# Kernel tuning notes

Hardware: AMD Instinct MI355X
Metric: run time of the kernel (lower is better)

Reference implementation:

```python
import jax, jax.numpy as jnp
import numpy as np

C = 256
CQK = C // 8  # query/key channel dim from Conv3d(in, in//8, 1)


def setup_inputs() -> dict:
    key = jax.random.key(0)
    ks = jax.random.split(key, 8)
    B, D, H, W = 2, 16, 16, 16
    x = jax.random.normal(ks[0], (B, C, D, H, W), dtype=jnp.float32)
    s = 1.0 / np.sqrt(C)
    q_w = jax.random.normal(ks[1], (CQK, C), dtype=jnp.float32) * s
    q_b = jax.random.normal(ks[2], (CQK,), dtype=jnp.float32) * 0.01
    k_w = jax.random.normal(ks[3], (CQK, C), dtype=jnp.float32) * s
    k_b = jax.random.normal(ks[4], (CQK,), dtype=jnp.float32) * 0.01
    v_w = jax.random.normal(ks[5], (C, C), dtype=jnp.float32) * s
    v_b = jax.random.normal(ks[6], (C,), dtype=jnp.float32) * 0.01
    gamma = jax.random.normal(ks[7], (1,), dtype=jnp.float32)
    return {"x": x, "q_w": q_w, "q_b": q_b, "k_w": k_w, "k_b": k_b,
            "v_w": v_w, "v_b": v_b, "gamma": gamma}


def reference(x, q_w, q_b, k_w, k_b, v_w, v_b, gamma):
    B, Cc, D, H, W = x.shape
    N = D * H * W
    xf = x.reshape(B, Cc, N)  # [B, C, N]
    # 1x1x1 Conv3d == channel-mixing matmul
    q = jnp.einsum('oc,bcn->bon', q_w, xf) + q_b[None, :, None]  # [B, C/8, N]
    k = jnp.einsum('oc,bcn->bon', k_w, xf) + k_b[None, :, None]  # [B, C/8, N]
    v = jnp.einsum('oc,bcn->bon', v_w, xf) + v_b[None, :, None]  # [B, C, N]
    # attention[b, i, j] = sum_c q[b, c, i] * k[b, c, j]
    attn = jnp.einsum('bci,bcj->bij', q, k)  # [B, N, N]
    attn = jax.nn.softmax(attn, axis=-1)
    # out[b, c, i] = sum_j v[b, c, j] * attn[b, i, j]
    out = jnp.einsum('bcj,bij->bci', v, attn)  # [B, C, N]
    out = out.reshape(B, Cc, D, H, W)
    return gamma[0] * out + x
```

## Files before the change

### kernel.cpp

```cpp
#include <hip/hip_runtime.h>

#define C_DIM 256
#define CQK   32
#define N_DIM 4096
#define B_DIM 2

typedef __attribute__((ext_vector_type(8))) short bf16x8;
typedef __attribute__((ext_vector_type(4))) float f32x4;

__device__ __forceinline__ unsigned short f2bf(float f) {
    union { float f; unsigned u; } v; v.f = f;
    unsigned r = v.u + 0x7FFFu + ((v.u >> 16) & 1u);
    return (unsigned short)(r >> 16);
}
__device__ __forceinline__ unsigned pk2(float a, float b) {
    return (unsigned)f2bf(a) | ((unsigned)f2bf(b) << 16);
}
__device__ __forceinline__ unsigned pk2t(float a, float b) {
    union { float f; unsigned u; } ua, ub; ua.f = a; ub.f = b;
    return __builtin_amdgcn_perm(ub.u, ua.u, 0x07060302u);
}
#define EXP2(x) __builtin_amdgcn_exp2f(x)
#define MFMA(A, B, C) __builtin_amdgcn_mfma_f32_16x16x32_bf16((A), (B), (C), 0, 0, 0)

__global__ __launch_bounds__(256) void wconv(
    const float* __restrict__ q_w, const float* __restrict__ q_b,
    const float* __restrict__ k_w, const float* __restrict__ k_b,
    const float* __restrict__ v_w, const float* __restrict__ v_b,
    unsigned short* __restrict__ wbf, float* __restrict__ biasf)
{
    const float LOG2E = 1.4426950408889634f;
    int o = blockIdx.x, c = threadIdx.x;
    float w;
    if (o < 32)       w = q_w[o * C_DIM + c] * LOG2E;
    else if (o < 64)  w = k_w[(o - 32) * C_DIM + c];
    else              w = v_w[(o - 64) * C_DIM + c];
    wbf[o * C_DIM + c] = f2bf(w);
    if (c == 0) biasf[o] = (o < 32) ? q_b[o] * LOG2E
                         : (o < 64) ? k_b[o - 32] : v_b[o - 64];
}

__global__ __launch_bounds__(256, 2) void qkv_proj(
    const float* __restrict__ x, const unsigned short* __restrict__ wbf,
    const float* __restrict__ biasf,
    unsigned short* __restrict__ qT, unsigned short* __restrict__ kT,
    unsigned short* __restrict__ vbf)
{
    __shared__ __align__(16) unsigned short xsT[16 * 264];
    __shared__ __align__(16) unsigned short qkbuf[2][16 * 36];
    __shared__ __align__(16) unsigned short vbb[256 * 20];
    const int t  = threadIdx.x;
    const int b  = blockIdx.x >> 8;
    const int n0 = (blockIdx.x & 255) * 16;

    {
        int n4 = t & 3, cq = t >> 2;
        const float* xp = x + ((size_t)(b * C_DIM + cq * 4)) * N_DIM + n0 + n4 * 4;
        float4 r0 = *(const float4*)xp;
        float4 r1 = *(const float4*)(xp + N_DIM);
        float4 r2 = *(const float4*)(xp + 2 * N_DIM);
        float4 r3 = *(const float4*)(xp + 3 * N_DIM);
        float a0[4], a1[4], a2[4], a3[4];
        *(float4*)a0 = r0; *(float4*)a1 = r1; *(float4*)a2 = r2; *(float4*)a3 = r3;
        #pragma unroll
        for (int k = 0; k < 4; ++k) {
            uint2 pw;
            pw.x = pk2(a0[k], a1[k]);
            pw.y = pk2(a2[k], a3[k]);
            *(uint2*)&xsT[(n4 * 4 + k) * 264 + cq * 4] = pw;
        }
    }
    __syncthreads();

    const int w = t >> 6, lid = t & 63, lr = lid & 15, lq = lid >> 4;
    f32x4 acc[5] = {};
    #pragma unroll
    for (int ks = 0; ks < 8; ++ks) {
        bf16x8 xb = *(const bf16x8*)&xsT[lr * 264 + ks * 32 + lq * 8];
        #pragma unroll
        for (int u = 0; u < 5; ++u) {
            int gm = w * 5 + u;
            bf16x8 af = *(const bf16x8*)&wbf[(gm * 16 + lr) * C_DIM + ks * 32 + lq * 8];
            acc[u] = MFMA(af, xb, acc[u]);
        }
    }
    #pragma unroll
    for (int u = 0; u < 5; ++u) {
        int gm = w * 5 + u;
        float bv[4];
        *(float4*)bv = *(const float4*)&biasf[gm * 16 + lq * 4];
        if (gm >= 4) {
            int vc = (gm - 4) * 16 + lq * 4;
            #pragma unroll
            for (int r = 0; r < 4; ++r)
                vbb[(vc + r) * 20 + lr] = f2bf(acc[u][r] + bv[r]);
        } else {
            int sel = gm >> 1, half = gm & 1;
            uint2 pw;
            pw.x = pk2(acc[u][0] + bv[0], acc[u][1] + bv[1]);
            pw.y = pk2(acc[u][2] + bv[2], acc[u][3] + bv[3]);
            *(uint2*)&qkbuf[sel][lr * 36 + half * 16 + lq * 4] = pw;
        }
    }
    __syncthreads();
    if (t < 128) {
        int sel = t >> 6, idx = t & 63;
        int n = idx >> 2, ch8 = (idx & 3) * 8;
        const unsigned short* src = &qkbuf[sel][n * 36 + ch8];
        uint2 a = *(const uint2*)src;
        uint2 c = *(const uint2*)(src + 4);
        unsigned short* dst = (sel ? kT : qT) + ((size_t)b * N_DIM + n0 + n) * CQK + ch8;
        uint4 st; st.x = a.x; st.y = a.y; st.z = c.x; st.w = c.y;
        *(uint4*)dst = st;
    }
    {
        const unsigned short* src = &vbb[t * 20];
        uint2 a = *(const uint2*)(src + 0);
        uint2 bq = *(const uint2*)(src + 4);
        uint2 c = *(const uint2*)(src + 8);
        uint2 d = *(const uint2*)(src + 12);
        unsigned short* dst = vbf + ((size_t)b * C_DIM + t) * N_DIM + n0;
        uint4 s0; s0.x = a.x; s0.y = a.y; s0.z = bq.x; s0.w = bq.y;
        uint4 s1; s1.x = c.x; s1.y = c.y; s1.z = d.x; s1.w = d.y;
        *(uint4*)dst = s0;
        *(uint4*)(dst + 8) = s1;
    }
}

__global__ __launch_bounds__(256, 2) void attn_kernel(
    const unsigned short* __restrict__ qT, const unsigned short* __restrict__ kT,
    const unsigned short* __restrict__ vbf, const float* __restrict__ x,
    const float* __restrict__ gamma, float* __restrict__ out)
{
    __shared__ __align__(16) char smem[40960 + 1536];
    unsigned short* pbase = (unsigned short*)smem;
    float* obuf = (float*)smem;
    float* lbuf = (float*)(smem + 40960);

    const int t  = threadIdx.x;
    const int b  = blockIdx.x >> 8;
    const int qt = (blockIdx.x >> 2) & 63;
    const int cs = blockIdx.x & 3;
    const int i0 = qt * 64, c0 = cs * 64;
    const int w = t >> 6, lid = t & 63, lr = lid & 15, lq = lid >> 4;

    const unsigned short* qTb = qT + (size_t)b * N_DIM * CQK;
    const unsigned short* kTb = kT + (size_t)b * N_DIM * CQK;
    const unsigned short* vb  = vbf + (size_t)b * C_DIM * N_DIM;

    unsigned short* pW0 = pbase + (w * 2 + 0) * (64 * 40);
    unsigned short* pW1 = pbase + (w * 2 + 1) * (64 * 40);

    bf16x8 bq[4];
    #pragma unroll
    for (int it = 0; it < 4; ++it)
        bq[it] = *(const bf16x8*)&qTb[(i0 + it * 16 + lr) * CQK + lq * 8];

    f32x4 oa[4][4] = {};
    float lp[4] = {};

    const int jwbase = w * 1024;

    bf16x8 akc0 = *(const bf16x8*)&kTb[(jwbase + lr) * CQK + lq * 8];
    bf16x8 akc1 = *(const bf16x8*)&kTb[(jwbase + 16 + lr) * CQK + lq * 8];
    bf16x8 avU[4];

    {
        #pragma unroll
        for (int ct = 0; ct < 4; ++ct)
            avU[ct] = *(const bf16x8*)&vb[(size_t)(c0 + ct * 16 + lr) * N_DIM + jwbase + lq * 8];
        bf16x8 akn0 = *(const bf16x8*)&kTb[(jwbase + 32 + lr) * CQK + lq * 8];
        bf16x8 akn1 = *(const bf16x8*)&kTb[(jwbase + 32 + 16 + lr) * CQK + lq * 8];
        const f32x4 z = {};
        #pragma unroll
        for (int it = 0; it < 4; ++it) {
            f32x4 s0 = MFMA(akc0, bq[it], z);
            f32x4 s1 = MFMA(akc1, bq[it], z);
            float e0 = EXP2(s0[0]), e1 = EXP2(s0[1]), e2 = EXP2(s0[2]), e3 = EXP2(s0[3]);
            float f0 = EXP2(s1[0]), f1 = EXP2(s1[1]), f2 = EXP2(s1[2]), f3 = EXP2(s1[3]);
            lp[it] += ((e0 + e1) + (e2 + e3)) + ((f0 + f1) + (f2 + f3));
            uint2 pw0; pw0.x = pk2t(e0, e1); pw0.y = pk2t(e2, e3);
            uint2 pw1; pw1.x = pk2t(f0, f1); pw1.y = pk2t(f2, f3);
            unsigned short* prow = pW0 + (it * 16 + lr) * 40;
            *(uint2*)&prow[lq * 4]      = pw0;
            *(uint2*)&prow[16 + lq * 4] = pw1;
        }
        akc0 = akn0; akc1 = akn1;
    }

    #pragma unroll 2
    for (int k = 1; k < 32; ++k) {
        const int j0 = jwbase + k * 32;
        const int jn = jwbase + ((k + 1) & 31) * 32;
        bf16x8 avI[4];
        #pragma unroll
        for (int ct = 0; ct < 4; ++ct)
            avI[ct] = *(const bf16x8*)&vb[(size_t)(c0 + ct * 16 + lr) * N_DIM + j0 + lq * 8];
        bf16x8 akn0 = *(const bf16x8*)&kTb[(jn + lr) * CQK + lq * 8];
        bf16x8 akn1 = *(const bf16x8*)&kTb[(jn + 16 + lr) * CQK + lq * 8];
        const unsigned short* pR = (k & 1) ? pW0 : pW1;
        bf16x8 bp[4];
        #pragma unroll
        for (int it = 0; it < 4; ++it)
            bp[it] = *(const bf16x8*)&pR[(it * 16 + lr) * 40 + lq * 8];
        const f32x4 z = {};
        f32x4 s[4][2];
        #pragma unroll
        for (int it = 0; it < 4; ++it) {
            s[it][0] = MFMA(akc0, bq[it], z);
            s[it][1] = MFMA(akc1, bq[it], z);
        }
        #pragma unroll
        for (int it = 0; it < 4; ++it)
            #pragma unroll
            for (int ct = 0; ct < 4; ++ct)
                oa[ct][it] = MFMA(avU[ct], bp[it], oa[ct][it]);
        unsigned short* pWc = (k & 1) ? pW1 : pW0;
        #pragma unroll
        for (int it = 0; it < 4; ++it) {
            float e0 = EXP2(s[it][0][0]), e1 = EXP2(s[it][0][1]);
            float e2 = EXP2(s[it][0][2]), e3 = EXP2(s[it][0][3]);
            float f0 = EXP2(s[it][1][0]), f1 = EXP2(s[it][1][1]);
            float f2 = EXP2(s[it][1][2]), f3 = EXP2(s[it][1][3]);
            lp[it] += ((e0 + e1) + (e2 + e3)) + ((f0 + f1) + (f2 + f3));
            uint2 pw0; pw0.x = pk2t(e0, e1); pw0.y = pk2t(e2, e3);
            uint2 pw1; pw1.x = pk2t(f0, f1); pw1.y = pk2t(f2, f3);
            unsigned short* prow = pWc + (it * 16 + lr) * 40;
            *(uint2*)&prow[lq * 4]      = pw0;
            *(uint2*)&prow[16 + lq * 4] = pw1;
        }
        akc0 = akn0; akc1 = akn1;
        #pragma unroll
        for (int ct = 0; ct < 4; ++ct) avU[ct] = avI[ct];
    }

    {
        bf16x8 bp[4];
        #pragma unroll
        for (int it = 0; it < 4; ++it)
            bp[it] = *(const bf16x8*)&pW1[(it * 16 + lr) * 40 + lq * 8];
        #pragma unroll
        for (int it = 0; it < 4; ++it)
            #pragma unroll
            for (int ct = 0; ct < 4; ++ct)
                oa[ct][it] = MFMA(avU[ct], bp[it], oa[ct][it]);
    }

    #pragma unroll
    for (int it = 0; it < 4; ++it) {
        lp[it] += __shfl_xor(lp[it], 16);
        lp[it] += __shfl_xor(lp[it], 32);
    }
    if (lq == 0) {
        #pragma unroll
        for (int it = 0; it < 4; ++it)
            lbuf[w * 64 + it * 16 + lr] = lp[it];
    }
    __syncthreads();

    for (int ph = 0; ph < 4; ++ph) {
        if (w == ph) {
            #pragma unroll
            for (int ct = 0; ct < 4; ++ct)
                #pragma unroll
                for (int it = 0; it < 4; ++it)
                    #pragma unroll
                    for (int r = 0; r < 4; ++r) {
                        int addr = (ct * 16 + lq * 4 + r) * 68 + it * 16 + lr;
                        if (ph == 0) obuf[addr]  = oa[ct][it][r];
                        else         obuf[addr] += oa[ct][it][r];
                    }
        }
        __syncthreads();
    }
    if (t < 64) {
        float l = lbuf[t] + lbuf[64 + t] + lbuf[128 + t] + lbuf[192 + t];
        lbuf[256 + t] = 1.f / l;
    }
    __syncthreads();

    const float g = gamma[0];
    const int cc = t >> 2;
    const int ic = (t & 3) * 16;
    const size_t rowbase = ((size_t)b * C_DIM + c0 + cc) * N_DIM + i0 + ic;
    #pragma unroll
    for (int k = 0; k < 4; ++k) {
        float4 ov4 = *(const float4*)&obuf[cc * 68 + ic + k * 4];
        float4 li  = *(const float4*)&lbuf[256 + ic + k * 4];
        float4 xv  = *(const float4*)(x + rowbase + k * 4);
        float4 ov;
        ov.x = g * ov4.x * li.x + xv.x;
        ov.y = g * ov4.y * li.y + xv.y;
        ov.z = g * ov4.z * li.z + xv.z;
        ov.w = g * ov4.w * li.w + xv.w;
        *(float4*)(out + rowbase + k * 4) = ov;
    }
}

extern "C" void kernel_launch(void* const* d_in, const int* in_sizes, int n_in,
                              void* d_out, int out_size, void* d_ws, size_t ws_size,
                              hipStream_t stream) {
    const float* x     = (const float*)d_in[0];
    const float* q_w   = (const float*)d_in[1];
    const float* q_b   = (const float*)d_in[2];
    const float* k_w   = (const float*)d_in[3];
    const float* k_b   = (const float*)d_in[4];
    const float* v_w   = (const float*)d_in[5];
    const float* v_b   = (const float*)d_in[6];
    const float* gamma = (const float*)d_in[7];
    float* out = (float*)d_out;

    char* ws = (char*)d_ws;
    unsigned short* qT    = (unsigned short*)(ws);
    unsigned short* kT    = (unsigned short*)(ws + 524288);
    unsigned short* vbf   = (unsigned short*)(ws + 1048576);
    unsigned short* wbf   = (unsigned short*)(ws + 5242880);
    float*          biasf = (float*)(ws + 5406720);

    hipLaunchKernelGGL(wconv, dim3(320), dim3(256), 0, stream,
                       q_w, q_b, k_w, k_b, v_w, v_b, wbf, biasf);
    hipLaunchKernelGGL(qkv_proj, dim3(B_DIM * 256), dim3(256), 0, stream,
                       x, wbf, biasf, qT, kT, vbf);
    hipLaunchKernelGGL(attn_kernel, dim3(B_DIM * 64 * 4), dim3(256), 0, stream,
                       qT, kT, vbf, x, gamma, out);
}
```

Baseline: 132.1 us.

## Fuse weight conversion, QKV projection and attention into one cooperative kernel

Merges the three kernel launches (weight bf16 conversion, QKV projection, attention) into a single cooperative-groups mega kernel with 512 blocks, separated by grid-wide syncs. This removes two kernel launch gaps and their inter-kernel drain/fill time. In exchange it adds grid.sync overhead and requires all 512 blocks to be co-resident, with a fallback to the old three-kernel path if the cooperative launch fails.

```diff
diff --git a/kernel.cpp b/kernel.cpp
--- a/kernel.cpp
+++ b/kernel.cpp
@@ -1,4 +1,7 @@
 #include <hip/hip_runtime.h>
+#include <hip/hip_cooperative_groups.h>
+
+namespace cg = cooperative_groups;
 
 #define C_DIM 256
 #define CQK   32
@@ -297,6 +300,283 @@
     }
 }
 
+__global__ __launch_bounds__(256, 2) void mega_kernel(
+    const float* __restrict__ x,
+    const float* __restrict__ q_w, const float* __restrict__ q_b,
+    const float* __restrict__ k_w, const float* __restrict__ k_b,
+    const float* __restrict__ v_w, const float* __restrict__ v_b,
+    const float* __restrict__ gamma, float* __restrict__ out,
+    unsigned short* __restrict__ qT, unsigned short* __restrict__ kT,
+    unsigned short* __restrict__ vbf, unsigned short* __restrict__ wbf,
+    float* __restrict__ biasf)
+{
+    __shared__ __align__(16) char smem[42496];
+    cg::grid_group grid = cg::this_grid();
+    const int bid = blockIdx.x;
+    const int t   = threadIdx.x;
+
+    if (bid < 320) {
+        const float LOG2E = 1.4426950408889634f;
+        int o = bid, c = t;
+        float w;
+        if (o < 32)       w = q_w[o * C_DIM + c] * LOG2E;
+        else if (o < 64)  w = k_w[(o - 32) * C_DIM + c];
+        else              w = v_w[(o - 64) * C_DIM + c];
+        wbf[o * C_DIM + c] = f2bf(w);
+        if (c == 0) biasf[o] = (o < 32) ? q_b[o] * LOG2E
+                             : (o < 64) ? k_b[o - 32] : v_b[o - 64];
+    }
+    __threadfence();
+    grid.sync();
+
+    {
+        unsigned short* xsT   = (unsigned short*)smem;
+        unsigned short* qkbuf = (unsigned short*)(smem + 8448);
+        unsigned short* vbb   = (unsigned short*)(smem + 10752);
+        const int b  = bid >> 8;
+        const int n0 = (bid & 255) * 16;
+
+        {
+            int n4 = t & 3, cq = t >> 2;
+            const float* xp = x + ((size_t)(b * C_DIM + cq * 4)) * N_DIM + n0 + n4 * 4;
+            float4 r0 = *(const float4*)xp;
+            float4 r1 = *(const float4*)(xp + N_DIM);
+            float4 r2 = *(const float4*)(xp + 2 * N_DIM);
+            float4 r3 = *(const float4*)(xp + 3 * N_DIM);
+            float a0[4], a1[4], a2[4], a3[4];
+            *(float4*)a0 = r0; *(float4*)a1 = r1; *(float4*)a2 = r2; *(float4*)a3 = r3;
+            #pragma unroll
+            for (int k = 0; k < 4; ++k) {
+                uint2 pw;
+                pw.x = pk2(a0[k], a1[k]);
+                pw.y = pk2(a2[k], a3[k]);
+                *(uint2*)&xsT[(n4 * 4 + k) * 264 + cq * 4] = pw;
+            }
+        }
+        __syncthreads();
+
+        const int w = t >> 6, lid = t & 63, lr = lid & 15, lq = lid >> 4;
+        f32x4 acc[5] = {};
+        #pragma unroll
+        for (int ks = 0; ks < 8; ++ks) {
+            bf16x8 xb = *(const bf16x8*)&xsT[lr * 264 + ks * 32 + lq * 8];
+            #pragma unroll
+            for (int u = 0; u < 5; ++u) {
+                int gm = w * 5 + u;
+                bf16x8 af = *(const bf16x8*)&wbf[(gm * 16 + lr) * C_DIM + ks * 32 + lq * 8];
+                acc[u] = MFMA(af, xb, acc[u]);
+            }
+        }
+        #pragma unroll
+        for (int u = 0; u < 5; ++u) {
+            int gm = w * 5 + u;
+            float bv[4];
+            *(float4*)bv = *(const float4*)&biasf[gm * 16 + lq * 4];
+            if (gm >= 4) {
+                int vc = (gm - 4) * 16 + lq * 4;
+                #pragma unroll
+                for (int r = 0; r < 4; ++r)
+                    vbb[(vc + r) * 20 + lr] = f2bf(acc[u][r] + bv[r]);
+            } else {
+                int sel = gm >> 1, half = gm & 1;
+                uint2 pw;
+                pw.x = pk2(acc[u][0] + bv[0], acc[u][1] + bv[1]);
+                pw.y = pk2(acc[u][2] + bv[2], acc[u][3] + bv[3]);
+                *(uint2*)&qkbuf[sel * 576 + lr * 36 + half * 16 + lq * 4] = pw;
+            }
+        }
+        __syncthreads();
+        if (t < 128) {
+            int sel = t >> 6, idx = t & 63;
+            int n = idx >> 2, ch8 = (idx & 3) * 8;
+            const unsigned short* src = &qkbuf[sel * 576 + n * 36 + ch8];
+            uint2 a = *(const uint2*)src;
+            uint2 c = *(const uint2*)(src + 4);
+            unsigned short* dst = (sel ? kT : qT) + ((size_t)b * N_DIM + n0 + n) * CQK + ch8;
+            uint4 st; st.x = a.x; st.y = a.y; st.z = c.x; st.w = c.y;
+            *(uint4*)dst = st;
+        }
+        {
+            const unsigned short* src = &vbb[t * 20];
+            uint2 a = *(const uint2*)(src + 0);
+            uint2 bq = *(const uint2*)(src + 4);
+            uint2 c = *(const uint2*)(src + 8);
+            uint2 d = *(const uint2*)(src + 12);
+            unsigned short* dst = vbf + ((size_t)b * C_DIM + t) * N_DIM + n0;
+            uint4 s0; s0.x = a.x; s0.y = a.y; s0.z = bq.x; s0.w = bq.y;
+            uint4 s1; s1.x = c.x; s1.y = c.y; s1.z = d.x; s1.w = d.y;
+            *(uint4*)dst = s0;
+            *(uint4*)(dst + 8) = s1;
+        }
+    }
+    __threadfence();
+    grid.sync();
+
+    {
+        unsigned short* pbase = (unsigned short*)smem;
+        float* obuf = (float*)smem;
+        float* lbuf = (float*)(smem + 40960);
+
+        const int b  = bid >> 8;
+        const int qt = (bid >> 2) & 63;
+        const int cs = bid & 3;
+        const int i0 = qt * 64, c0 = cs * 64;
+        const int w = t >> 6, lid = t & 63, lr = lid & 15, lq = lid >> 4;
+
+        const unsigned short* qTb = qT + (size_t)b * N_DIM * CQK;
+        const unsigned short* kTb = kT + (size_t)b * N_DIM * CQK;
+        const unsigned short* vb  = vbf + (size_t)b * C_DIM * N_DIM;
+
+        unsigned short* pW0 = pbase + (w * 2 + 0) * (64 * 40);
+        unsigned short* pW1 = pbase + (w * 2 + 1) * (64 * 40);
+
+        bf16x8 bq[4];
+        #pragma unroll
+        for (int it = 0; it < 4; ++it)
+            bq[it] = *(const bf16x8*)&qTb[(i0 + it * 16 + lr) * CQK + lq * 8];
+
+        f32x4 oa[4][4] = {};
+        float lp[4] = {};
+
+        const int jwbase = w * 1024;
+
+        bf16x8 akc0 = *(const bf16x8*)&kTb[(jwbase + lr) * CQK + lq * 8];
+        bf16x8 akc1 = *(const bf16x8*)&kTb[(jwbase + 16 + lr) * CQK + lq * 8];
+        bf16x8 avU[4];
+
+        {
+            #pragma unroll
+            for (int ct = 0; ct < 4; ++ct)
+                avU[ct] = *(const bf16x8*)&vb[(size_t)(c0 + ct * 16 + lr) * N_DIM + jwbase + lq * 8];
+            bf16x8 akn0 = *(const bf16x8*)&kTb[(jwbase + 32 + lr) * CQK + lq * 8];
+            bf16x8 akn1 = *(const bf16x8*)&kTb[(jwbase + 32 + 16 + lr) * CQK + lq * 8];
+            const f32x4 z = {};
+            #pragma unroll
+            for (int it = 0; it < 4; ++it) {
+                f32x4 s0 = MFMA(akc0, bq[it], z);
+                f32x4 s1 = MFMA(akc1, bq[it], z);
+                float e0 = EXP2(s0[0]), e1 = EXP2(s0[1]), e2 = EXP2(s0[2]), e3 = EXP2(s0[3]);
+                float f0 = EXP2(s1[0]), f1 = EXP2(s1[1]), f2 = EXP2(s1[2]), f3 = EXP2(s1[3]);
+                lp[it] += ((e0 + e1) + (e2 + e3)) + ((f0 + f1) + (f2 + f3));
+                uint2 pw0; pw0.x = pk2t(e0, e1); pw0.y = pk2t(e2, e3);
+                uint2 pw1; pw1.x = pk2t(f0, f1); pw1.y = pk2t(f2, f3);
+                unsigned short* prow = pW0 + (it * 16 + lr) * 40;
+                *(uint2*)&prow[lq * 4]      = pw0;
+                *(uint2*)&prow[16 + lq * 4] = pw1;
+            }
+            akc0 = akn0; akc1 = akn1;
+        }
+
+        #pragma unroll 2
+        for (int k = 1; k < 32; ++k) {
+            const int j0 = jwbase + k * 32;
+            const int jn = jwbase + ((k + 1) & 31) * 32;
+            bf16x8 avI[4];
+            #pragma unroll
+            for (int ct = 0; ct < 4; ++ct)
+                avI[ct] = *(const bf16x8*)&vb[(size_t)(c0 + ct * 16 + lr) * N_DIM + j0 + lq * 8];
+            bf16x8 akn0 = *(const bf16x8*)&kTb[(jn + lr) * CQK + lq * 8];
+            bf16x8 akn1 = *(const bf16x8*)&kTb[(jn + 16 + lr) * CQK + lq * 8];
+            const unsigned short* pR = (k & 1) ? pW0 : pW1;
+            bf16x8 bp[4];
+            #pragma unroll
+            for (int it = 0; it < 4; ++it)
+                bp[it] = *(const bf16x8*)&pR[(it * 16 + lr) * 40 + lq * 8];
+            const f32x4 z = {};
+            f32x4 s[4][2];
+            #pragma unroll
+            for (int it = 0; it < 4; ++it) {
+                s[it][0] = MFMA(akc0, bq[it], z);
+                s[it][1] = MFMA(akc1, bq[it], z);
+            }
+            #pragma unroll
+            for (int it = 0; it < 4; ++it)
+                #pragma unroll
+                for (int ct = 0; ct < 4; ++ct)
+                    oa[ct][it] = MFMA(avU[ct], bp[it], oa[ct][it]);
+            unsigned short* pWc = (k & 1) ? pW1 : pW0;
+            #pragma unroll
+            for (int it = 0; it < 4; ++it) {
+                float e0 = EXP2(s[it][0][0]), e1 = EXP2(s[it][0][1]);
+                float e2 = EXP2(s[it][0][2]), e3 = EXP2(s[it][0][3]);
+                float f0 = EXP2(s[it][1][0]), f1 = EXP2(s[it][1][1]);
+                float f2 = EXP2(s[it][1][2]), f3 = EXP2(s[it][1][3]);
+                lp[it] += ((e0 + e1) + (e2 + e3)) + ((f0 + f1) + (f2 + f3));
+                uint2 pw0; pw0.x = pk2t(e0, e1); pw0.y = pk2t(e2, e3);
+                uint2 pw1; pw1.x = pk2t(f0, f1); pw1.y = pk2t(f2, f3);
+                unsigned short* prow = pWc + (it * 16 + lr) * 40;
+                *(uint2*)&prow[lq * 4]      = pw0;
+                *(uint2*)&prow[16 + lq * 4] = pw1;
+            }
+            akc0 = akn0; akc1 = akn1;
+            #pragma unroll
+            for (int ct = 0; ct < 4; ++ct) avU[ct] = avI[ct];
+        }
+
+        {
+            bf16x8 bp[4];
+            #pragma unroll
+            for (int it = 0; it < 4; ++it)
+                bp[it] = *(const bf16x8*)&pW1[(it * 16 + lr) * 40 + lq * 8];
+            #pragma unroll
+            for (int it = 0; it < 4; ++it)
+                #pragma unroll
+                for (int ct = 0; ct < 4; ++ct)
+                    oa[ct][it] = MFMA(avU[ct], bp[it], oa[ct][it]);
+        }
+
+        #pragma unroll
+        for (int it = 0; it < 4; ++it) {
+            lp[it] += __shfl_xor(lp[it], 16);
+            lp[it] += __shfl_xor(lp[it], 32);
+        }
+        if (lq == 0) {
+            #pragma unroll
+            for (int it = 0; it < 4; ++it)
+                lbuf[w * 64 + it * 16 + lr] = lp[it];
+        }
+        __syncthreads();
+
+        for (int ph = 0; ph < 4; ++ph) {
+            if (w == ph) {
+                #pragma unroll
+                for (int ct = 0; ct < 4; ++ct)
+                    #pragma unroll
+                    for (int it = 0; it < 4; ++it)
+                        #pragma unroll
+                        for (int r = 0; r < 4; ++r) {
+                            int addr = (ct * 16 + lq * 4 + r) * 68 + it * 16 + lr;
+                            if (ph == 0) obuf[addr]  = oa[ct][it][r];
+                            else         obuf[addr] += oa[ct][it][r];
+                        }
+            }
+            __syncthreads();
+        }
+        if (t < 64) {
+            float l = lbuf[t] + lbuf[64 + t] + lbuf[128 + t] + lbuf[192 + t];
+            lbuf[256 + t] = 1.f / l;
+        }
+        __syncthreads();
+
+        const float g = gamma[0];
+        const int cc = t >> 2;
+        const int ic = (t & 3) * 16;
+        const size_t rowbase = ((size_t)b * C_DIM + c0 + cc) * N_DIM + i0 + ic;
+        #pragma unroll
+        for (int k = 0; k < 4; ++k) {
+            float4 ov4 = *(const float4*)&obuf[cc * 68 + ic + k * 4];
+            float4 li  = *(const float4*)&lbuf[256 + ic + k * 4];
+            float4 xv  = *(const float4*)(x + rowbase + k * 4);
+            float4 ov;
+            ov.x = g * ov4.x * li.x + xv.x;
+            ov.y = g * ov4.y * li.y + xv.y;
+            ov.z = g * ov4.z * li.z + xv.z;
+            ov.w = g * ov4.w * li.w + xv.w;
+            *(float4*)(out + rowbase + k * 4) = ov;
+        }
+    }
+}
+
 extern "C" void kernel_launch(void* const* d_in, const int* in_sizes, int n_in,
                               void* d_out, int out_size, void* d_ws, size_t ws_size,
                               hipStream_t stream) {
@@ -317,10 +597,21 @@
     unsigned short* wbf   = (unsigned short*)(ws + 5242880);
     float*          biasf = (float*)(ws + 5406720);
 
-    hipLaunchKernelGGL(wconv, dim3(320), dim3(256), 0, stream,
-                       q_w, q_b, k_w, k_b, v_w, v_b, wbf, biasf);
-    hipLaunchKernelGGL(qkv_proj, dim3(B_DIM * 256), dim3(256), 0, stream,
-                       x, wbf, biasf, qT, kT, vbf);
-    hipLaunchKernelGGL(attn_kernel, dim3(B_DIM * 64 * 4), dim3(256), 0, stream,
-                       qT, kT, vbf, x, gamma, out);
-}
+    void* args[] = {
+        (void*)&x, (void*)&q_w, (void*)&q_b, (void*)&k_w, (void*)&k_b,
+        (void*)&v_w, (void*)&v_b, (void*)&gamma, (void*)&out,
+        (void*)&qT, (void*)&kT, (void*)&vbf, (void*)&wbf, (void*)&biasf
+    };
+    hipError_t err = hipLaunchCooperativeKernel((const void*)mega_kernel,
+                                                dim3(512), dim3(256),
+                                                args, 0, stream);
+    if (err != hipSuccess) {
+        (void)hipGetLastError();
+        hipLaunchKernelGGL(wconv, dim3(320), dim3(256), 0, stream,
+                           q_w, q_b, k_w, k_b, v_w, v_b, wbf, biasf);
+        hipLaunchKernelGGL(qkv_proj, dim3(B_DIM * 256), dim3(256), 0, stream,
+                           x, wbf, biasf, qT, kT, vbf);
+        hipLaunchKernelGGL(attn_kernel, dim3(B_DIM * 64 * 4), dim3(256), 0, stream,
+                           qT, kT, vbf, x, gamma, out);
+    }
+}
```

Result: slower. 337.0 us (+155.1%).
